# Kernel optimization log

Hardware: AMD Instinct MI355X
Metric: run time of the kernel (lower is better)

## Reference

```python
import jax, jax.numpy as jnp
import numpy as np

N_NODES = 100000
N_REL = 3
N_EDGES = 400000
D = 128


def setup_inputs() -> dict:
    key = jax.random.key(0)
    k_x, k_e, k_w = jax.random.split(key, 3)
    x = jax.random.normal(k_x, (N_NODES, D), dtype=jnp.float32)
    edges = jax.random.randint(k_e, (N_REL, 2, N_EDGES), 0, N_NODES, dtype=jnp.int64)
    # GraphConv weight per relation (glorot-ish scale) and bias
    W = jax.random.normal(k_w, (N_REL, D, D), dtype=jnp.float32) / np.sqrt(D)
    b = jnp.zeros((N_REL, D), dtype=jnp.float32)
    return {"x": x, "edges": edges, "W": W, "b": b}


def reference(x, edges, W, b):
    """HetGraphLayer with GCN convs per edge type, mean channel-combine.

    Each relation: dgl GraphConv with norm='both':
      out = D_in^{-1/2} * A^T * (D_out^{-1/2} * x @ W) + b
    with degrees clamped to min 1 (allow_zero_in_degree=True).
    """
    N = x.shape[0]

    def per_rel(e, Wr, br):
        src, dst = e[0], e[1]  # [E]
        ones = jnp.ones(src.shape, dtype=x.dtype)
        deg_out = jnp.maximum(jax.ops.segment_sum(ones, src, num_segments=N), 1.0)
        deg_in = jnp.maximum(jax.ops.segment_sum(ones, dst, num_segments=N), 1.0)
        h = (x * jax.lax.rsqrt(deg_out)[:, None]) @ Wr          # [N, D]
        agg = jax.ops.segment_sum(h[src], dst, num_segments=N)  # [N, D]
        return agg * jax.lax.rsqrt(deg_in)[:, None] + br

    rel_embs = jax.vmap(per_rel)(edges, W, b)  # [R, N, D] (torch.stack over etypes)
    return jnp.mean(rel_embs, axis=0)          # ChannelCombine 'mean'
```

## Files before the change

### kernel.cpp

```cpp
#include <hip/hip_runtime.h>
#include <hip/hip_fp16.h>
#include <math.h>

#define N_NODES 100000
#define N_RELS  3
#define N_EDGES 400000
#define D       128
#define NTOT    (N_RELS * N_NODES)
#define ELL_W   12
#define OVF_CAP 4096
#define BSH     9
#define NB      196
#define BCAP    3072
#define CHUNK   4096
#define NCH     98
#define PASS1_BLKS (NCH * N_RELS)
#define XH_BLKS 1024
#define GEMM_BLKS 782

typedef _Float16 f16x8 __attribute__((ext_vector_type(8)));
typedef float    f32x4 __attribute__((ext_vector_type(4)));

static __device__ __forceinline__ ushort f2h(float f) {
    return __builtin_bit_cast(ushort, (_Float16)f);
}
static __device__ __forceinline__ float h_lo(uint u) {
    return __low2float(__builtin_bit_cast(__half2, u));
}
static __device__ __forceinline__ float h_hi(uint u) {
    return __high2float(__builtin_bit_cast(__half2, u));
}

__global__ void prep_w_kernel(const float* __restrict__ W, const float* __restrict__ b,
                              ushort* __restrict__ Wt, float* __restrict__ bsum) {
    int id = blockIdx.x * 256 + threadIdx.x;
    if (id < 3 * D * D) {
        int r = id >> 14;
        int rem = id & 16383;
        int k = rem >> 7, j = rem & 127;
        Wt[r * 16384 + j * 128 + k] = f2h(W[id]);
    }
    if (blockIdx.x == 0 && threadIdx.x < D) {
        int j = threadIdx.x;
        bsum[j] = (b[j] + b[D + j] + b[2 * D + j]) * (1.0f / 3.0f);
    }
}

__global__ __launch_bounds__(256) void pass1_kernel(
    const float* __restrict__ x, const int* __restrict__ edges,
    ushort* __restrict__ xh,
    int* __restrict__ part_dst, int* __restrict__ part_src,
    int* __restrict__ gcur_dst, int* __restrict__ gcur_src) {
    __shared__ struct { int s[CHUNK]; int t[CHUNK]; } st;
    __shared__ int histd[NB], hists[NB], segd[NB], segs[NB];
    const int bid = blockIdx.x;
    const int tid = threadIdx.x;

    if (bid < PASS1_BLKS) {
        const int rel   = bid / NCH;
        const int chunk = bid - rel * NCH;
        const int e0 = chunk * CHUNK;
        const int ne = min(CHUNK, N_EDGES - e0);
        const int* src = edges + (size_t)(rel * 2 + 0) * N_EDGES;
        const int* dst = edges + (size_t)(rel * 2 + 1) * N_EDGES;

        for (int i = tid; i < NB; i += 256) { histd[i] = 0; hists[i] = 0; }
        __syncthreads();
        for (int i = tid; i < ne; i += 256) {
            int s = src[e0 + i], t = dst[e0 + i];
            st.s[i] = s; st.t[i] = t;
            atomicAdd(&histd[t >> BSH], 1);
            atomicAdd(&hists[s >> BSH], 1);
        }
        __syncthreads();
        for (int i = tid; i < NB; i += 256) {
            int hd = histd[i];
            segd[i] = hd ? atomicAdd(&gcur_dst[rel * NB + i], hd) : 0;
            int hs = hists[i];
            segs[i] = hs ? atomicAdd(&gcur_src[rel * NB + i], hs) : 0;
            histd[i] = 0; hists[i] = 0;
        }
        __syncthreads();
        for (int i = tid; i < ne; i += 256) {
            int s = st.s[i], t = st.t[i];
            int bd = t >> BSH;
            int p = segd[bd] + atomicAdd(&histd[bd], 1);
            if (p < BCAP)
                part_dst[(size_t)(rel * NB + bd) * BCAP + p] = (s << 9) | (t & 511);
            int bs = s >> BSH;
            int q = segs[bs] + atomicAdd(&hists[bs], 1);
            if (q < BCAP) part_src[(size_t)(rel * NB + bs) * BCAP + q] = s;
        }
    } else {
        const int ngrp = N_NODES * D / 8;
        for (int i = (bid - PASS1_BLKS) * 256 + tid; i < ngrp; i += XH_BLKS * 256) {
            const float4* xp = (const float4*)x + 2 * (size_t)i;
            float4 a = xp[0], bq = xp[1];
            uint4 v;
            v.x = (uint)f2h(a.x)  | ((uint)f2h(a.y)  << 16);
            v.y = (uint)f2h(a.z)  | ((uint)f2h(a.w)  << 16);
            v.z = (uint)f2h(bq.x) | ((uint)f2h(bq.y) << 16);
            v.w = (uint)f2h(bq.z) | ((uint)f2h(bq.w) << 16);
            ((uint4*)xh)[i] = v;
        }
    }
}

__global__ __launch_bounds__(256) void pass2a_kernel(
    const int* __restrict__ part_src, const int* __restrict__ gcur_src,
    float* __restrict__ rdo) {
    __shared__ int cnt[512];
    const int b = blockIdx.x, rel = blockIdx.y;
    const int tid = threadIdx.x;
    const int n0 = b << BSH;
    const int nvalid = min(512, N_NODES - n0);
    for (int i = tid; i < 512; i += 256) cnt[i] = 0;
    __syncthreads();
    const int m = min(gcur_src[rel * NB + b], BCAP);
    const int* ps = part_src + (size_t)(rel * NB + b) * BCAP;
    for (int i = tid; i < m; i += 256) atomicAdd(&cnt[ps[i] & 511], 1);
    __syncthreads();
    for (int i = tid; i < nvalid; i += 256)
        rdo[rel * N_NODES + n0 + i] = rsqrtf((float)max(cnt[i], 1));
}

__global__ __launch_bounds__(1024) void agg_kernel(
    const int* __restrict__ part_dst, const int* __restrict__ gcur_dst,
    const ushort* __restrict__ xh, const float* __restrict__ rdo,
    float* __restrict__ rdi, ushort* __restrict__ agg,
    int* __restrict__ ovf_cnt, int2* __restrict__ ovf) {
    __shared__ int cnt[512];
    __shared__ int lell[512 * ELL_W];
    const int b = blockIdx.x, rel = blockIdx.y;
    const int tid = threadIdx.x;
    const int n0 = b << BSH;
    const int nvalid = min(512, N_NODES - n0);

    if (tid < 512) cnt[tid] = 0;
    __syncthreads();
    const int m = min(gcur_dst[rel * NB + b], BCAP);
    const int* pp = part_dst + (size_t)(rel * NB + b) * BCAP;
    for (int i = tid; i < m; i += 1024) {
        int pd = pp[i];
        int s = ((unsigned)pd) >> 9;
        int li = pd & 511;
        int p = atomicAdd(&cnt[li], 1);
        if (p < ELL_W) lell[li * ELL_W + p] = s;
        else {
            int o = atomicAdd(ovf_cnt, 1);
            if (o < OVF_CAP) ovf[o] = make_int2(s, (n0 + li) | (rel << 20));
        }
    }
    __syncthreads();
    if (tid < nvalid)
        rdi[rel * N_NODES + n0 + tid] = rsqrtf((float)max(cnt[tid], 1));

    const int w = tid >> 6, l = tid & 63;
    for (int it = 0; it < 32; ++it) {
        int li = w * 32 + it;
        int n = n0 + li;
        if (n >= N_NODES) break;
        int full = cnt[li];
        int c = min(full, ELL_W);
        int e = 0; float cl = 0.f;
        if (l < c) {
            e = lell[li * ELL_W + l];
            cl = rdo[rel * N_NODES + e];
        }
        float ax = 0.f, ay = 0.f;
        int i = 0;
        for (; i + 2 <= c; i += 2) {
            int s0 = __shfl(e, i), s1 = __shfl(e, i + 1);
            float c0 = __shfl(cl, i), c1 = __shfl(cl, i + 1);
            uint u0 = *(const uint*)(xh + (size_t)s0 * 128 + 2 * l);
            uint u1 = *(const uint*)(xh + (size_t)s1 * 128 + 2 * l);
            ax = fmaf(h_lo(u0), c0, ax);
            ay = fmaf(h_hi(u0), c0, ay);
            ax = fmaf(h_lo(u1), c1, ax);
            ay = fmaf(h_hi(u1), c1, ay);
        }
        if (i < c) {
            int s0 = __shfl(e, i);
            float c0 = __shfl(cl, i);
            uint u0 = *(const uint*)(xh + (size_t)s0 * 128 + 2 * l);
            ax = fmaf(h_lo(u0), c0, ax);
            ay = fmaf(h_hi(u0), c0, ay);
        }
        float rv = rsqrtf((float)max(full, 1));
        ax *= rv; ay *= rv;
        uint pk = (uint)f2h(ax) | ((uint)f2h(ay) << 16);
        *(uint*)(agg + ((size_t)rel * N_NODES + n) * 128 + 2 * l) = pk;
    }
}

__global__ __launch_bounds__(256) void gemm_kernel(
    const ushort* __restrict__ agg, const ushort* __restrict__ Wt,
    const float* __restrict__ bsum, float* __restrict__ out) {
    __shared__ ushort Bt[128 * 128];
    const int n0 = blockIdx.x * 128;
    const int tid = threadIdx.x;
    const int w = tid >> 6, l = tid & 63;
    const int wrow = w * 32;
    const int lr = l & 15, lk = (l >> 4) * 8;

    f32x4 acc[2][8];
    #pragma unroll
    for (int fi = 0; fi < 2; ++fi)
        #pragma unroll
        for (int fj = 0; fj < 8; ++fj)
            acc[fi][fj] = (f32x4){0.f, 0.f, 0.f, 0.f};

    for (int rel = 0; rel < 3; ++rel) {
        __syncthreads();
        {
            const ushort* Wg = Wt + rel * 16384;
            #pragma unroll
            for (int c = 0; c < 8; ++c) {
                int id = c * 256 + tid;
                int j = id >> 4, k8 = id & 15;
                uint4 v = *(const uint4*)(Wg + j * 128 + k8 * 8);
                int ba = (j * 256 + k8 * 16) ^ ((j & 7) << 4);
                *(uint4*)((char*)Bt + ba) = v;
            }
        }
        __syncthreads();

        f16x8 a[2][4];
        #pragma unroll
        for (int fi = 0; fi < 2; ++fi) {
            int row = min(n0 + wrow + fi * 16 + lr, N_NODES - 1);
            const ushort* ap = agg + ((size_t)rel * N_NODES + row) * 128 + lk;
            #pragma unroll
            for (int ks = 0; ks < 4; ++ks)
                a[fi][ks] = *(const f16x8*)(ap + ks * 32);
        }

        #pragma unroll
        for (int ks = 0; ks < 4; ++ks) {
            f16x8 bfr[8];
            #pragma unroll
            for (int fj = 0; fj < 8; ++fj) {
                int j = fj * 16 + lr;
                int ba = (j * 256 + (ks * 32 + lk) * 2) ^ ((j & 7) << 4);
                bfr[fj] = *(f16x8*)((char*)Bt + ba);
            }
            #pragma unroll
            for (int fi = 0; fi < 2; ++fi)
                #pragma unroll
                for (int fj = 0; fj < 8; ++fj)
                    acc[fi][fj] = __builtin_amdgcn_mfma_f32_16x16x32_f16(
                        a[fi][ks], bfr[fj], acc[fi][fj], 0, 0, 0);
        }
    }

    const int cr4 = (l >> 4) * 4;
    #pragma unroll
    for (int fi = 0; fi < 2; ++fi) {
        int rbase = n0 + wrow + fi * 16 + cr4;
        #pragma unroll
        for (int fj = 0; fj < 8; ++fj) {
            int col = fj * 16 + lr;
            float bs = bsum[col];
            #pragma unroll
            for (int i = 0; i < 4; ++i) {
                int row = rbase + i;
                if (row < N_NODES)
                    out[(size_t)row * 128 + col] = acc[fi][fj][i] * (1.f / 3.f) + bs;
            }
        }
    }
}

__global__ void ovf_kernel(const ushort* __restrict__ xh, const ushort* __restrict__ Wt,
                           const float* __restrict__ rdi, const float* __restrict__ rdo,
                           const int* __restrict__ ovf_cnt, const int2* __restrict__ ovf,
                           float* out) {
    int m = min(*ovf_cnt, OVF_CAP);
    int wid = (blockIdx.x * blockDim.x + threadIdx.x) >> 6;
    int l = threadIdx.x & 63;
    int nw = (gridDim.x * blockDim.x) >> 6;
    for (int ent = wid; ent < m; ent += nw) {
        int s = ovf[ent].x;
        int packed = ovf[ent].y;
        int t = packed & 0xFFFFF, r = packed >> 20;
        uint myx = *(const uint*)(xh + (size_t)s * 128 + 2 * l);
        const ushort* w0 = Wt + r * 16384 + (2 * l) * 128;
        const ushort* w1 = w0 + 128;
        float a0 = 0.f, a1 = 0.f;
        for (int kk = 0; kk < 64; ++kk) {
            uint xu = __shfl(myx, kk);
            float x0 = h_lo(xu), x1 = h_hi(xu);
            uint wa = *(const uint*)(w0 + 2 * kk);
            uint wb = *(const uint*)(w1 + 2 * kk);
            a0 += x0 * h_lo(wa) + x1 * h_hi(wa);
            a1 += x0 * h_lo(wb) + x1 * h_hi(wb);
        }
        float sc = rdo[r * N_NODES + s] * rdi[r * N_NODES + t] * (1.f / 3.f);
        atomicAdd(out + (size_t)t * 128 + 2 * l + 0, a0 * sc);
        atomicAdd(out + (size_t)t * 128 + 2 * l + 1, a1 * sc);
    }
}

extern "C" void kernel_launch(void* const* d_in, const int* in_sizes, int n_in,
                              void* d_out, int out_size, void* d_ws, size_t ws_size,
                              hipStream_t stream) {
    const float* x     = (const float*)d_in[0];
    const int*   edges = (const int*)d_in[1];
    const float* W     = (const float*)d_in[2];
    const float* b     = (const float*)d_in[3];
    float* out = (float*)d_out;

    char* ws = (char*)d_ws;
    size_t off = 0;
    auto alloc = [&](size_t bytes) -> void* {
        void* p = ws + off;
        off += (bytes + 255) & ~(size_t)255;
        return p;
    };
    int*   gcur_dst = (int*)alloc((size_t)N_RELS * NB * 4);
    int*   gcur_src = (int*)alloc((size_t)N_RELS * NB * 4);
    int*   ovf_cnt  = (int*)alloc(256);
    size_t zero_bytes = off;
    float* bsum     = (float*)alloc((size_t)D * 4);
    ushort* Wt      = (ushort*)alloc((size_t)3 * D * D * 2);
    int2*  ovf      = (int2*)alloc((size_t)OVF_CAP * 8);
    int*   part_dst = (int*)alloc((size_t)N_RELS * NB * BCAP * 4);
    int*   part_src = (int*)alloc((size_t)N_RELS * NB * BCAP * 4);
    float* rdi      = (float*)alloc((size_t)NTOT * 4);
    float* rdo      = (float*)alloc((size_t)NTOT * 4);
    ushort* xh      = (ushort*)alloc((size_t)N_NODES * D * 2);
    ushort* agg     = (ushort*)alloc((size_t)N_RELS * N_NODES * D * 2);

    hipMemsetAsync(ws, 0, zero_bytes, stream);
    prep_w_kernel<<<192, 256, 0, stream>>>(W, b, Wt, bsum);
    pass1_kernel<<<PASS1_BLKS + XH_BLKS, 256, 0, stream>>>(
        x, edges, xh, part_dst, part_src, gcur_dst, gcur_src);
    pass2a_kernel<<<dim3(NB, 3), 256, 0, stream>>>(part_src, gcur_src, rdo);
    agg_kernel<<<dim3(NB, 3), 1024, 0, stream>>>(
        part_dst, gcur_dst, xh, rdo, rdi, agg, ovf_cnt, ovf);
    gemm_kernel<<<GEMM_BLKS, 256, 0, stream>>>(agg, Wt, bsum, out);
    ovf_kernel<<<16, 256, 0, stream>>>(xh, Wt, rdi, rdo, ovf_cnt, ovf, out);
}
```

Before: 176.4 us.

## Fuse gather-aggregation into GEMM kernel via shared-memory tile, merge degree passes

Aggregation of neighbor features now happens inside the GEMM kernel. Each block gathers its 128 rows per relation into a swizzled LDS tile and feeds them straight to MFMA, so the fp16 agg buffer (3×N×D) is no longer written to and read back from global memory. The ELL build and both degree counts are merged into one pass2 kernel, which writes the ELL lists and raw in-degrees to global memory. The cost is extra global ELL traffic and far fewer blocks doing the gather (782 blocks of 512 threads rather than 588 blocks of 1024). Gather latency is now also serialized with the MFMA work inside each block.

```diff
diff --git a/kernel.cpp b/kernel.cpp
--- a/kernel.cpp
+++ b/kernel.cpp
@@ -16,7 +16,7 @@
 #define NCH     98
 #define PASS1_BLKS (NCH * N_RELS)
 #define XH_BLKS 1024
-#define GEMM_BLKS 782
+#define MEGA_BLKS 782
 
 typedef _Float16 f16x8 __attribute__((ext_vector_type(8)));
 typedef float    f32x4 __attribute__((ext_vector_type(4)));
@@ -106,28 +106,10 @@
     }
 }
 
-__global__ __launch_bounds__(256) void pass2a_kernel(
-    const int* __restrict__ part_src, const int* __restrict__ gcur_src,
-    float* __restrict__ rdo) {
-    __shared__ int cnt[512];
-    const int b = blockIdx.x, rel = blockIdx.y;
-    const int tid = threadIdx.x;
-    const int n0 = b << BSH;
-    const int nvalid = min(512, N_NODES - n0);
-    for (int i = tid; i < 512; i += 256) cnt[i] = 0;
-    __syncthreads();
-    const int m = min(gcur_src[rel * NB + b], BCAP);
-    const int* ps = part_src + (size_t)(rel * NB + b) * BCAP;
-    for (int i = tid; i < m; i += 256) atomicAdd(&cnt[ps[i] & 511], 1);
-    __syncthreads();
-    for (int i = tid; i < nvalid; i += 256)
-        rdo[rel * N_NODES + n0 + i] = rsqrtf((float)max(cnt[i], 1));
-}
-
-__global__ __launch_bounds__(1024) void agg_kernel(
-    const int* __restrict__ part_dst, const int* __restrict__ gcur_dst,
-    const ushort* __restrict__ xh, const float* __restrict__ rdo,
-    float* __restrict__ rdi, ushort* __restrict__ agg,
+__global__ __launch_bounds__(256) void pass2_kernel(
+    const int* __restrict__ part_dst, const int* __restrict__ part_src,
+    const int* __restrict__ gcur_dst, const int* __restrict__ gcur_src,
+    int* __restrict__ ell, int* __restrict__ deg_in, float* __restrict__ rdo,
     int* __restrict__ ovf_cnt, int2* __restrict__ ovf) {
     __shared__ int cnt[512];
     __shared__ int lell[512 * ELL_W];
@@ -136,11 +118,11 @@
     const int n0 = b << BSH;
     const int nvalid = min(512, N_NODES - n0);
 
-    if (tid < 512) cnt[tid] = 0;
+    for (int i = tid; i < 512; i += 256) cnt[i] = 0;
     __syncthreads();
     const int m = min(gcur_dst[rel * NB + b], BCAP);
     const int* pp = part_dst + (size_t)(rel * NB + b) * BCAP;
-    for (int i = tid; i < m; i += 1024) {
+    for (int i = tid; i < m; i += 256) {
         int pd = pp[i];
         int s = ((unsigned)pd) >> 9;
         int li = pd & 511;
@@ -152,88 +134,87 @@
         }
     }
     __syncthreads();
-    if (tid < nvalid)
-        rdi[rel * N_NODES + n0 + tid] = rsqrtf((float)max(cnt[tid], 1));
-
-    const int w = tid >> 6, l = tid & 63;
-    for (int it = 0; it < 32; ++it) {
-        int li = w * 32 + it;
-        int n = n0 + li;
-        if (n >= N_NODES) break;
-        int full = cnt[li];
-        int c = min(full, ELL_W);
-        int e = 0; float cl = 0.f;
-        if (l < c) {
-            e = lell[li * ELL_W + l];
-            cl = rdo[rel * N_NODES + e];
-        }
-        float ax = 0.f, ay = 0.f;
-        int i = 0;
-        for (; i + 2 <= c; i += 2) {
-            int s0 = __shfl(e, i), s1 = __shfl(e, i + 1);
-            float c0 = __shfl(cl, i), c1 = __shfl(cl, i + 1);
-            uint u0 = *(const uint*)(xh + (size_t)s0 * 128 + 2 * l);
-            uint u1 = *(const uint*)(xh + (size_t)s1 * 128 + 2 * l);
-            ax = fmaf(h_lo(u0), c0, ax);
-            ay = fmaf(h_hi(u0), c0, ay);
-            ax = fmaf(h_lo(u1), c1, ax);
-            ay = fmaf(h_hi(u1), c1, ay);
-        }
-        if (i < c) {
-            int s0 = __shfl(e, i);
-            float c0 = __shfl(cl, i);
-            uint u0 = *(const uint*)(xh + (size_t)s0 * 128 + 2 * l);
-            ax = fmaf(h_lo(u0), c0, ax);
-            ay = fmaf(h_hi(u0), c0, ay);
-        }
-        float rv = rsqrtf((float)max(full, 1));
-        ax *= rv; ay *= rv;
-        uint pk = (uint)f2h(ax) | ((uint)f2h(ay) << 16);
-        *(uint*)(agg + ((size_t)rel * N_NODES + n) * 128 + 2 * l) = pk;
-    }
-}
-
-__global__ __launch_bounds__(256) void gemm_kernel(
-    const ushort* __restrict__ agg, const ushort* __restrict__ Wt,
-    const float* __restrict__ bsum, float* __restrict__ out) {
+    for (int i = tid; i < nvalid; i += 256)
+        deg_in[rel * N_NODES + n0 + i] = cnt[i];
+    for (int i = tid; i < nvalid * ELL_W; i += 256)
+        ell[(size_t)(rel * N_NODES + n0) * ELL_W + i] = lell[i];
+    __syncthreads();
+    for (int i = tid; i < 512; i += 256) cnt[i] = 0;
+    __syncthreads();
+    const int m2 = min(gcur_src[rel * NB + b], BCAP);
+    const int* ps = part_src + (size_t)(rel * NB + b) * BCAP;
+    for (int i = tid; i < m2; i += 256) atomicAdd(&cnt[ps[i] & 511], 1);
+    __syncthreads();
+    for (int i = tid; i < nvalid; i += 256)
+        rdo[rel * N_NODES + n0 + i] = rsqrtf((float)max(cnt[i], 1));
+}
+
+__global__ __launch_bounds__(512) void mega_kernel(
+    const ushort* __restrict__ xh, const ushort* __restrict__ Wt,
+    const int* __restrict__ ell, const int* __restrict__ deg_in,
+    const float* __restrict__ rdo, const float* __restrict__ bsum,
+    float* __restrict__ out) {
     __shared__ ushort Bt[128 * 128];
+    __shared__ ushort tile[128 * 128];
     const int n0 = blockIdx.x * 128;
     const int tid = threadIdx.x;
     const int w = tid >> 6, l = tid & 63;
-    const int wrow = w * 32;
     const int lr = l & 15, lk = (l >> 4) * 8;
 
-    f32x4 acc[2][8];
+    f32x4 acc[8];
     #pragma unroll
-    for (int fi = 0; fi < 2; ++fi)
-        #pragma unroll
-        for (int fj = 0; fj < 8; ++fj)
-            acc[fi][fj] = (f32x4){0.f, 0.f, 0.f, 0.f};
+    for (int fj = 0; fj < 8; ++fj) acc[fj] = (f32x4){0.f, 0.f, 0.f, 0.f};
 
     for (int rel = 0; rel < 3; ++rel) {
         __syncthreads();
         {
             const ushort* Wg = Wt + rel * 16384;
             #pragma unroll
-            for (int c = 0; c < 8; ++c) {
-                int id = c * 256 + tid;
+            for (int c = 0; c < 4; ++c) {
+                int id = c * 512 + tid;
                 int j = id >> 4, k8 = id & 15;
                 uint4 v = *(const uint4*)(Wg + j * 128 + k8 * 8);
                 int ba = (j * 256 + k8 * 16) ^ ((j & 7) << 4);
                 *(uint4*)((char*)Bt + ba) = v;
             }
         }
-        __syncthreads();
-
-        f16x8 a[2][4];
-        #pragma unroll
-        for (int fi = 0; fi < 2; ++fi) {
-            int row = min(n0 + wrow + fi * 16 + lr, N_NODES - 1);
-            const ushort* ap = agg + ((size_t)rel * N_NODES + row) * 128 + lk;
-            #pragma unroll
-            for (int ks = 0; ks < 4; ++ks)
-                a[fi][ks] = *(const f16x8*)(ap + ks * 32);
-        }
+        for (int it = 0; it < 16; ++it) {
+            int li = w * 16 + it;
+            int n = n0 + li;
+            int base = rel * N_NODES + min(n, N_NODES - 1);
+            int full = (n < N_NODES) ? deg_in[base] : 0;
+            int c = min(full, ELL_W);
+            int e = 0; float cl = 0.f;
+            if (l < c) {
+                e = ell[(size_t)base * ELL_W + l];
+                cl = rdo[rel * N_NODES + e];
+            }
+            float ax = 0.f, ay = 0.f;
+            int i = 0;
+            for (; i + 2 <= c; i += 2) {
+                int s0 = __shfl(e, i), s1 = __shfl(e, i + 1);
+                float c0 = __shfl(cl, i), c1 = __shfl(cl, i + 1);
+                uint u0 = *(const uint*)(xh + (size_t)s0 * 128 + 2 * l);
+                uint u1 = *(const uint*)(xh + (size_t)s1 * 128 + 2 * l);
+                ax = fmaf(h_lo(u0), c0, ax);
+                ay = fmaf(h_hi(u0), c0, ay);
+                ax = fmaf(h_lo(u1), c1, ax);
+                ay = fmaf(h_hi(u1), c1, ay);
+            }
+            if (i < c) {
+                int s0 = __shfl(e, i);
+                float c0 = __shfl(cl, i);
+                uint u0 = *(const uint*)(xh + (size_t)s0 * 128 + 2 * l);
+                ax = fmaf(h_lo(u0), c0, ax);
+                ay = fmaf(h_hi(u0), c0, ay);
+            }
+            float rv = rsqrtf((float)max(full, 1));
+            ax *= rv; ay *= rv;
+            uint pk = (uint)f2h(ax) | ((uint)f2h(ay) << 16);
+            int ba = (li * 256 + 4 * l) ^ ((li & 7) << 4);
+            *(uint*)((char*)tile + ba) = pk;
+        }
+        __syncthreads();
 
         #pragma unroll
         for (int ks = 0; ks < 4; ++ks) {
@@ -244,35 +225,33 @@
                 int ba = (j * 256 + (ks * 32 + lk) * 2) ^ ((j & 7) << 4);
                 bfr[fj] = *(f16x8*)((char*)Bt + ba);
             }
+            int row = w * 16 + lr;
+            int ba = (row * 256 + (ks * 32 + lk) * 2) ^ ((row & 7) << 4);
+            f16x8 afr = *(f16x8*)((char*)tile + ba);
             #pragma unroll
-            for (int fi = 0; fi < 2; ++fi)
-                #pragma unroll
-                for (int fj = 0; fj < 8; ++fj)
-                    acc[fi][fj] = __builtin_amdgcn_mfma_f32_16x16x32_f16(
-                        a[fi][ks], bfr[fj], acc[fi][fj], 0, 0, 0);
+            for (int fj = 0; fj < 8; ++fj)
+                acc[fj] = __builtin_amdgcn_mfma_f32_16x16x32_f16(
+                    afr, bfr[fj], acc[fj], 0, 0, 0);
         }
     }
 
     const int cr4 = (l >> 4) * 4;
+    const int rbase = n0 + w * 16 + cr4;
     #pragma unroll
-    for (int fi = 0; fi < 2; ++fi) {
-        int rbase = n0 + wrow + fi * 16 + cr4;
+    for (int fj = 0; fj < 8; ++fj) {
+        int col = fj * 16 + lr;
+        float bs = bsum[col];
         #pragma unroll
-        for (int fj = 0; fj < 8; ++fj) {
-            int col = fj * 16 + lr;
-            float bs = bsum[col];
-            #pragma unroll
-            for (int i = 0; i < 4; ++i) {
-                int row = rbase + i;
-                if (row < N_NODES)
-                    out[(size_t)row * 128 + col] = acc[fi][fj][i] * (1.f / 3.f) + bs;
-            }
+        for (int i = 0; i < 4; ++i) {
+            int row = rbase + i;
+            if (row < N_NODES)
+                out[(size_t)row * 128 + col] = acc[fj][i] * (1.f / 3.f) + bs;
         }
     }
 }
 
 __global__ void ovf_kernel(const ushort* __restrict__ xh, const ushort* __restrict__ Wt,
-                           const float* __restrict__ rdi, const float* __restrict__ rdo,
+                           const int* __restrict__ deg_in, const float* __restrict__ rdo,
                            const int* __restrict__ ovf_cnt, const int2* __restrict__ ovf,
                            float* out) {
     int m = min(*ovf_cnt, OVF_CAP);
@@ -295,7 +274,8 @@
             a0 += x0 * h_lo(wa) + x1 * h_hi(wa);
             a1 += x0 * h_lo(wb) + x1 * h_hi(wb);
         }
-        float sc = rdo[r * N_NODES + s] * rdi[r * N_NODES + t] * (1.f / 3.f);
+        float rdi = rsqrtf((float)max(deg_in[r * N_NODES + t], 1));
+        float sc = rdo[r * N_NODES + s] * rdi * (1.f / 3.f);
         atomicAdd(out + (size_t)t * 128 + 2 * l + 0, a0 * sc);
         atomicAdd(out + (size_t)t * 128 + 2 * l + 1, a1 * sc);
     }
@@ -326,18 +306,18 @@
     int2*  ovf      = (int2*)alloc((size_t)OVF_CAP * 8);
     int*   part_dst = (int*)alloc((size_t)N_RELS * NB * BCAP * 4);
     int*   part_src = (int*)alloc((size_t)N_RELS * NB * BCAP * 4);
-    float* rdi      = (float*)alloc((size_t)NTOT * 4);
+    int*   ell      = (int*)alloc((size_t)NTOT * ELL_W * 4);
+    int*   deg_in   = (int*)alloc((size_t)NTOT * 4);
     float* rdo      = (float*)alloc((size_t)NTOT * 4);
     ushort* xh      = (ushort*)alloc((size_t)N_NODES * D * 2);
-    ushort* agg     = (ushort*)alloc((size_t)N_RELS * N_NODES * D * 2);
 
     hipMemsetAsync(ws, 0, zero_bytes, stream);
     prep_w_kernel<<<192, 256, 0, stream>>>(W, b, Wt, bsum);
     pass1_kernel<<<PASS1_BLKS + XH_BLKS, 256, 0, stream>>>(
         x, edges, xh, part_dst, part_src, gcur_dst, gcur_src);
-    pass2a_kernel<<<dim3(NB, 3), 256, 0, stream>>>(part_src, gcur_src, rdo);
-    agg_kernel<<<dim3(NB, 3), 1024, 0, stream>>>(
-        part_dst, gcur_dst, xh, rdo, rdi, agg, ovf_cnt, ovf);
-    gemm_kernel<<<GEMM_BLKS, 256, 0, stream>>>(agg, Wt, bsum, out);
-    ovf_kernel<<<16, 256, 0, stream>>>(xh, Wt, rdi, rdo, ovf_cnt, ovf, out);
-}
+    pass2_kernel<<<dim3(NB, 3), 256, 0, stream>>>(
+        part_dst, part_src, gcur_dst, gcur_src, ell, deg_in, rdo, ovf_cnt, ovf);
+    mega_kernel<<<MEGA_BLKS, 512, 0, stream>>>(
+        xh, Wt, ell, deg_in, rdo, bsum, out);
+    ovf_kernel<<<16, 256, 0, stream>>>(xh, Wt, deg_in, rdo, ovf_cnt, ovf, out);
+}
```

New measurement: 254.2 us. +44.1%, slower.
